# Performance work log

Hardware: AMD Instinct MI355X
Metric: run time of the kernel (lower is better)

## Reference

```python
import jax, jax.numpy as jnp
import numpy as np
import math

B, N, E, H = 2, 4096, 256, 8
HS = E // H  # head_size = 32


def setup_inputs() -> dict:
    key = jax.random.key(0)
    ks = jax.random.split(key, 8)
    s = 1.0 / math.sqrt(E)
    return {
        "node_features": jax.random.normal(ks[0], (B, N, E), dtype=jnp.float32),
        "adj": jax.random.randint(ks[1], (B, N, N), 0, 2).astype(jnp.bool_),
        "Wq": jax.random.normal(ks[2], (E, E), dtype=jnp.float32) * s,
        "bq": jax.random.normal(ks[3], (E,), dtype=jnp.float32) * s,
        "Wk": jax.random.normal(ks[4], (E, E), dtype=jnp.float32) * s,
        "bk": jax.random.normal(ks[5], (E,), dtype=jnp.float32) * s,
        "Wv": jax.random.normal(ks[6], (E, E), dtype=jnp.float32) * s,
        "bv": jax.random.normal(ks[7], (E,), dtype=jnp.float32) * s,
    }


def _split_heads(x):
    # (B, N, E) -> (B, H, N, HS)
    return x.reshape(B, N, H, HS).transpose(0, 2, 1, 3)


def reference(node_features, adj, Wq, bq, Wk, bk, Wv, bv):
    # nn.Linear: x @ W.T + b
    Q = _split_heads(node_features @ Wq.T + bq)
    K = _split_heads(node_features @ Wk.T + bk)
    V = _split_heads(node_features @ Wv.T + bv)
    scores = jnp.einsum("bhnd,bhmd->bhnm", Q, K) / math.sqrt(HS)
    scores = jnp.where(adj[:, None, :, :], scores, -jnp.inf)
    probs = jax.nn.softmax(scores, axis=-1)
    out = jnp.einsum("bhnm,bhmd->bhnd", probs, V)
    # (B, H, N, HS) -> (B, N, E); note: original forward does NOT apply W_out
    return out.transpose(0, 2, 1, 3).reshape(B, N, E)
```

## Files before the change

### kernel.cpp

```cpp
#include <hip/hip_runtime.h>

typedef __attribute__((ext_vector_type(8))) short short8;
typedef __attribute__((ext_vector_type(4))) float f32x4;
typedef __attribute__((ext_vector_type(4))) unsigned short u16x4;

constexpr int cB = 2, cN = 4096, cE = 256, cH = 8, cHS = 32;

__device__ __forceinline__ unsigned short f2bf(float f) {
    unsigned int u = __builtin_bit_cast(unsigned int, f);
    u = (u + 0x7FFFu + ((u >> 16) & 1u)) >> 16;
    return (unsigned short)u;
}

__device__ __forceinline__ unsigned int cvt_pk_bf16(float lo, float hi) {
    unsigned int r;
    asm("v_cvt_pk_bf16_f32 %0, %1, %2" : "=v"(r) : "v"(lo), "v"(hi));
    return r;
}

__global__ __launch_bounds__(256) void cvt_x_kernel(const float* __restrict__ x,
                                                    unsigned short* __restrict__ xb) {
    int t = blockIdx.x * 256 + threadIdx.x;
    f32x4 v = *((const f32x4*)x + t);
    u16x4 o = { f2bf(v[0]), f2bf(v[1]), f2bf(v[2]), f2bf(v[3]) };
    *((u16x4*)xb + t) = o;
}

__global__ __launch_bounds__(256) void cvt_w_kernel(const float* __restrict__ Wq,
                                                    const float* __restrict__ Wk,
                                                    const float* __restrict__ Wv,
                                                    unsigned short* __restrict__ wcb) {
    int t = blockIdx.x * 256 + threadIdx.x;
    int f = t * 4;
    int o = f >> 8, i = f & 255;
    const float* src = (o < 256) ? Wq : (o < 512 ? Wk : Wv);
    f32x4 v = *(const f32x4*)(src + (size_t)(o & 255) * 256 + i);
    u16x4 ov = { f2bf(v[0]), f2bf(v[1]), f2bf(v[2]), f2bf(v[3]) };
    *((u16x4*)wcb + t) = ov;
}

__global__ __launch_bounds__(256) void bitpack_kernel(const int* __restrict__ adj,
                                                      unsigned long long* __restrict__ mask) {
    int lane = threadIdx.x & 63;
    int wave = blockIdx.x * 4 + (threadIdx.x >> 6);
    const int nwaves = 2048 * 4;
    const int nwords = cB * cN * cN / 64;
    for (int w = wave; w < nwords; w += nwaves) {
        int v = adj[(size_t)w * 64 + lane];
        unsigned long long bal = __ballot(v != 0);
        if (lane == 0) mask[w] = bal;
    }
}

__global__ __launch_bounds__(256) void qkv_proj_kernel(const unsigned short* __restrict__ xb,
                                                       const unsigned short* __restrict__ wcb,
                                                       const float* __restrict__ bq,
                                                       const float* __restrict__ bk,
                                                       const float* __restrict__ bv,
                                                       unsigned short* __restrict__ Qb,
                                                       unsigned short* __restrict__ Kb,
                                                       unsigned short* __restrict__ Vt) {
    const int wv = threadIdx.x >> 6, lane = threadIdx.x & 63;
    const int col = lane & 15, grp = lane >> 4;
    const int rowbase = blockIdx.x * 64 + wv * 16;
    const int colbase = blockIdx.y * 64;
    f32x4 acc[4] = {};
    for (int kk = 0; kk < 8; ++kk) {
        short8 a = *(const short8*)(xb + (size_t)(rowbase + col) * 256 + kk * 32 + grp * 8);
        #pragma unroll
        for (int c = 0; c < 4; ++c) {
            short8 bf = *(const short8*)(wcb + (size_t)(colbase + c * 16 + col) * 256 + kk * 32 + grp * 8);
            acc[c] = __builtin_amdgcn_mfma_f32_16x16x32_bf16(a, bf, acc[c], 0, 0, 0);
        }
    }
    #pragma unroll
    for (int c = 0; c < 4; ++c) {
        const int o = colbase + c * 16 + col;
        const int sel = o >> 8, oo = o & 255;
        const float bias = (sel == 0 ? bq : sel == 1 ? bk : bv)[oo];
        const int h = oo >> 5, hs = oo & 31;
        const int R0 = rowbase + grp * 4;
        const int b = R0 >> 12, n0 = R0 & 4095;
        if (sel < 2) {
            unsigned short* dst = (sel == 0) ? Qb : Kb;
            #pragma unroll
            for (int r = 0; r < 4; ++r)
                dst[(size_t)((b * cH + h) * cN + n0 + r) * cHS + hs] = f2bf(acc[c][r] + bias);
        } else {
            unsigned short* vrow = Vt + (size_t)((b * cH + h) * cHS + hs) * cN;
            #pragma unroll
            for (int r = 0; r < 4; ++r) {
                const int n = n0 + r;
                const int pos = (n & ~31) + 2 * (n & 15) + ((n >> 4) & 1);
                vrow[pos] = f2bf(acc[c][r] + bias);
            }
        }
    }
}

__global__ __launch_bounds__(256) void attn_kernel(const unsigned short* __restrict__ Qb,
                                                   const unsigned short* __restrict__ Kb,
                                                   const unsigned short* __restrict__ Vt,
                                                   const unsigned int* __restrict__ mask32,
                                                   float* __restrict__ out) {
    __shared__ unsigned int p_smem[4][2][16][20];
    const int wv = threadIdx.x >> 6, lane = threadIdx.x & 63;
    const int col = lane & 15, grp = lane >> 4;
    int bid = blockIdx.x;
    bid = (bid & 7) * 64 + (bid >> 3);
    const int task = bid * 4 + wv;
    const int qt = task & 127, h = (task >> 7) & 7, b = task >> 10;
    const int qbase = qt * 32;
    const unsigned short* Qh = Qb + (size_t)(b * cH + h) * cN * cHS;
    const unsigned short* Kh = Kb + (size_t)(b * cH + h) * cN * cHS;
    const unsigned short* Vh = Vt + (size_t)(b * cH + h) * cHS * cN;
    const unsigned int* mrow = mask32 + (size_t)(b * cN + qbase) * 128;
    unsigned int (*pb)[16][20] = p_smem[wv];

    short8 aq[2];
    aq[0] = *(const short8*)(Qh + (size_t)(qbase + col) * cHS + grp * 8);
    aq[1] = *(const short8*)(Qh + (size_t)(qbase + 16 + col) * cHS + grp * 8);

    f32x4 acc[2][2] = {};
    float ll[2][4] = {};
    const float CE = 1.4426950408889634f * 0.17677669529663687f;
    const f32x4 z4 = {0.f, 0.f, 0.f, 0.f};

    short8 ck0 = *(const short8*)(Kh + (size_t)col * cHS + grp * 8);
    short8 ck1 = *(const short8*)(Kh + (size_t)(16 + col) * cHS + grp * 8);
    short8 cv0 = *(const short8*)(Vh + (size_t)col * cN + grp * 8);
    short8 cv1 = *(const short8*)(Vh + (size_t)(16 + col) * cN + grp * 8);
    unsigned int cm[8];
    #pragma unroll
    for (int i = 0; i < 8; ++i)
        cm[i] = mrow[(size_t)((i >> 2) * 16 + grp * 4 + (i & 3)) * 128];

    for (int kt = 0; kt < 128; ++kt) {
        const short8 k0 = ck0, k1 = ck1, v0 = cv0, v1 = cv1;
        unsigned int m8[8];
        #pragma unroll
        for (int i = 0; i < 8; ++i) m8[i] = cm[i];
        if (kt < 127) {
            const int kb = (kt + 1) * 32;
            ck0 = *(const short8*)(Kh + (size_t)(kb + col) * cHS + grp * 8);
            ck1 = *(const short8*)(Kh + (size_t)(kb + 16 + col) * cHS + grp * 8);
            cv0 = *(const short8*)(Vh + (size_t)col * cN + kb + grp * 8);
            cv1 = *(const short8*)(Vh + (size_t)(16 + col) * cN + kb + grp * 8);
            #pragma unroll
            for (int i = 0; i < 8; ++i)
                cm[i] = mrow[(size_t)((i >> 2) * 16 + grp * 4 + (i & 3)) * 128 + kt + 1];
        }

        f32x4 s[2][2];
        s[0][0] = __builtin_amdgcn_mfma_f32_16x16x32_bf16(aq[0], k0, z4, 0, 0, 0);
        s[0][1] = __builtin_amdgcn_mfma_f32_16x16x32_bf16(aq[0], k1, z4, 0, 0, 0);
        s[1][0] = __builtin_amdgcn_mfma_f32_16x16x32_bf16(aq[1], k0, z4, 0, 0, 0);
        s[1][1] = __builtin_amdgcn_mfma_f32_16x16x32_bf16(aq[1], k1, z4, 0, 0, 0);

        #pragma unroll
        for (int qs = 0; qs < 2; ++qs) {
            #pragma unroll
            for (int r = 0; r < 4; ++r) {
                const unsigned int w32 = m8[qs * 4 + r];
                float e0 = __builtin_exp2f(s[qs][0][r] * CE);
                float e1 = __builtin_exp2f(s[qs][1][r] * CE);
                e0 = ((w32 >> col) & 1u) ? e0 : 0.f;
                e1 = ((w32 >> (16 + col)) & 1u) ? e1 : 0.f;
                ll[qs][r] += e0 + e1;
                pb[qs][grp * 4 + r][col] = cvt_pk_bf16(e0, e1);
            }
        }
        #pragma unroll
        for (int qs = 0; qs < 2; ++qs) {
            short8 pa = *(const short8*)&pb[qs][col][grp * 4];
            acc[qs][0] = __builtin_amdgcn_mfma_f32_16x16x32_bf16(pa, v0, acc[qs][0], 0, 0, 0);
            acc[qs][1] = __builtin_amdgcn_mfma_f32_16x16x32_bf16(pa, v1, acc[qs][1], 0, 0, 0);
        }
    }

    #pragma unroll
    for (int qs = 0; qs < 2; ++qs) {
        #pragma unroll
        for (int r = 0; r < 4; ++r) {
            float s = ll[qs][r];
            s += __shfl_xor(s, 1);
            s += __shfl_xor(s, 2);
            s += __shfl_xor(s, 4);
            s += __shfl_xor(s, 8);
            const float inv = 1.0f / s;
            const int qrow = qbase + qs * 16 + grp * 4 + r;
            float* op = out + (size_t)(b * cN + qrow) * cE + h * 32;
            op[col]      = acc[qs][0][r] * inv;
            op[16 + col] = acc[qs][1][r] * inv;
        }
    }
}

extern "C" void kernel_launch(void* const* d_in, const int* in_sizes, int n_in,
                              void* d_out, int out_size, void* d_ws, size_t ws_size,
                              hipStream_t stream) {
    const float* x   = (const float*)d_in[0];
    const int*   adj = (const int*)d_in[1];
    const float* Wq  = (const float*)d_in[2];
    const float* bq  = (const float*)d_in[3];
    const float* Wk  = (const float*)d_in[4];
    const float* bk  = (const float*)d_in[5];
    const float* Wv  = (const float*)d_in[6];
    const float* bv  = (const float*)d_in[7];
    float* out = (float*)d_out;

    char* ws = (char*)d_ws;
    unsigned short* Xb  = (unsigned short*)(ws);
    unsigned short* Wcb = (unsigned short*)(ws + (4ull << 20));
    unsigned short* Qb  = (unsigned short*)(ws + (5ull << 20));
    unsigned short* Kb  = (unsigned short*)(ws + (9ull << 20));
    unsigned short* Vt  = (unsigned short*)(ws + (13ull << 20));
    unsigned long long* mask64 = (unsigned long long*)(ws + (17ull << 20));

    cvt_x_kernel<<<dim3(2048), dim3(256), 0, stream>>>(x, Xb);
    cvt_w_kernel<<<dim3(192), dim3(256), 0, stream>>>(Wq, Wk, Wv, Wcb);
    bitpack_kernel<<<dim3(2048), dim3(256), 0, stream>>>(adj, mask64);
    qkv_proj_kernel<<<dim3(128, 12), dim3(256), 0, stream>>>(Xb, Wcb, bq, bk, bv, Qb, Kb, Vt);
    attn_kernel<<<dim3(512), dim3(256), 0, stream>>>(Qb, Kb, Vt, (const unsigned int*)mask64, out);
}
```

Before: 196.1 us.

## Split key range across waves in attention and fold scaling into Q

Each attention block now handles one 32-query tile, and its four waves each take a quarter of the key range. Partial outputs and row sums are combined through shared memory, which quadruples the grid and adds parallelism. The softmax scale is folded into Q during projection, masking becomes a bitwise AND on packed bf16, and row sums are computed by an MFMA against a ones vector instead of scalar adds. The software prefetch of the next K/V/mask tile is removed and replaced with direct loads inside the loop, which risks exposing more memory latency.

```diff
diff --git a/kernel.cpp b/kernel.cpp
--- a/kernel.cpp
+++ b/kernel.cpp
@@ -64,6 +64,7 @@
     const int col = lane & 15, grp = lane >> 4;
     const int rowbase = blockIdx.x * 64 + wv * 16;
     const int colbase = blockIdx.y * 64;
+    const float CE = 1.4426950408889634f * 0.17677669529663687f;
     f32x4 acc[4] = {};
     for (int kk = 0; kk < 8; ++kk) {
         short8 a = *(const short8*)(xb + (size_t)(rowbase + col) * 256 + kk * 32 + grp * 8);
@@ -81,11 +82,14 @@
         const int h = oo >> 5, hs = oo & 31;
         const int R0 = rowbase + grp * 4;
         const int b = R0 >> 12, n0 = R0 & 4095;
-        if (sel < 2) {
-            unsigned short* dst = (sel == 0) ? Qb : Kb;
+        if (sel == 0) {
             #pragma unroll
             for (int r = 0; r < 4; ++r)
-                dst[(size_t)((b * cH + h) * cN + n0 + r) * cHS + hs] = f2bf(acc[c][r] + bias);
+                Qb[(size_t)((b * cH + h) * cN + n0 + r) * cHS + hs] = f2bf((acc[c][r] + bias) * CE);
+        } else if (sel == 1) {
+            #pragma unroll
+            for (int r = 0; r < 4; ++r)
+                Kb[(size_t)((b * cH + h) * cN + n0 + r) * cHS + hs] = f2bf(acc[c][r] + bias);
         } else {
             unsigned short* vrow = Vt + (size_t)((b * cH + h) * cHS + hs) * cN;
             #pragma unroll
@@ -98,101 +102,90 @@
     }
 }
 
-__global__ __launch_bounds__(256) void attn_kernel(const unsigned short* __restrict__ Qb,
-                                                   const unsigned short* __restrict__ Kb,
-                                                   const unsigned short* __restrict__ Vt,
-                                                   const unsigned int* __restrict__ mask32,
-                                                   float* __restrict__ out) {
-    __shared__ unsigned int p_smem[4][2][16][20];
+__global__ __launch_bounds__(256, 5) void attn_kernel(const unsigned short* __restrict__ Qb,
+                                                      const unsigned short* __restrict__ Kb,
+                                                      const unsigned short* __restrict__ Vt,
+                                                      const unsigned int* __restrict__ mask32,
+                                                      float* __restrict__ out) {
+    __shared__ float comb[4][64][24];
     const int wv = threadIdx.x >> 6, lane = threadIdx.x & 63;
     const int col = lane & 15, grp = lane >> 4;
     int bid = blockIdx.x;
-    bid = (bid & 7) * 64 + (bid >> 3);
-    const int task = bid * 4 + wv;
-    const int qt = task & 127, h = (task >> 7) & 7, b = task >> 10;
+    bid = (bid & 7) * 256 + (bid >> 3);
+    const int qt = bid & 127, h = (bid >> 7) & 7, b = bid >> 10;
     const int qbase = qt * 32;
     const unsigned short* Qh = Qb + (size_t)(b * cH + h) * cN * cHS;
     const unsigned short* Kh = Kb + (size_t)(b * cH + h) * cN * cHS;
     const unsigned short* Vh = Vt + (size_t)(b * cH + h) * cHS * cN;
     const unsigned int* mrow = mask32 + (size_t)(b * cN + qbase) * 128;
-    unsigned int (*pb)[16][20] = p_smem[wv];
-
-    short8 aq[2];
-    aq[0] = *(const short8*)(Qh + (size_t)(qbase + col) * cHS + grp * 8);
-    aq[1] = *(const short8*)(Qh + (size_t)(qbase + 16 + col) * cHS + grp * 8);
+    unsigned int* pw = (unsigned int*)&comb[0][0][0] + wv * 640;
+
+    const short8 aq0 = *(const short8*)(Qh + (size_t)(qbase + col) * cHS + grp * 8);
+    const short8 aq1 = *(const short8*)(Qh + (size_t)(qbase + 16 + col) * cHS + grp * 8);
 
     f32x4 acc[2][2] = {};
-    float ll[2][4] = {};
-    const float CE = 1.4426950408889634f * 0.17677669529663687f;
+    f32x4 lacc[2] = {};
     const f32x4 z4 = {0.f, 0.f, 0.f, 0.f};
-
-    short8 ck0 = *(const short8*)(Kh + (size_t)col * cHS + grp * 8);
-    short8 ck1 = *(const short8*)(Kh + (size_t)(16 + col) * cHS + grp * 8);
-    short8 cv0 = *(const short8*)(Vh + (size_t)col * cN + grp * 8);
-    short8 cv1 = *(const short8*)(Vh + (size_t)(16 + col) * cN + grp * 8);
-    unsigned int cm[8];
-    #pragma unroll
-    for (int i = 0; i < 8; ++i)
-        cm[i] = mrow[(size_t)((i >> 2) * 16 + grp * 4 + (i & 3)) * 128];
-
-    for (int kt = 0; kt < 128; ++kt) {
-        const short8 k0 = ck0, k1 = ck1, v0 = cv0, v1 = cv1;
-        unsigned int m8[8];
-        #pragma unroll
-        for (int i = 0; i < 8; ++i) m8[i] = cm[i];
-        if (kt < 127) {
-            const int kb = (kt + 1) * 32;
-            ck0 = *(const short8*)(Kh + (size_t)(kb + col) * cHS + grp * 8);
-            ck1 = *(const short8*)(Kh + (size_t)(kb + 16 + col) * cHS + grp * 8);
-            cv0 = *(const short8*)(Vh + (size_t)col * cN + kb + grp * 8);
-            cv1 = *(const short8*)(Vh + (size_t)(16 + col) * cN + kb + grp * 8);
-            #pragma unroll
-            for (int i = 0; i < 8; ++i)
-                cm[i] = mrow[(size_t)((i >> 2) * 16 + grp * 4 + (i & 3)) * 128 + kt + 1];
-        }
+    const short8 ones = { 0x3F80, 0x3F80, 0x3F80, 0x3F80, 0x3F80, 0x3F80, 0x3F80, 0x3F80 };
+
+    const int ktEnd = wv * 32 + 32;
+    #pragma unroll 1
+    for (int kt = wv * 32; kt < ktEnd; ++kt) {
+        const int kbase = kt * 32;
+        const short8 k0 = *(const short8*)(Kh + (size_t)(kbase + col) * cHS + grp * 8);
+        const short8 k1 = *(const short8*)(Kh + (size_t)(kbase + 16 + col) * cHS + grp * 8);
+        const short8 v0 = *(const short8*)(Vh + (size_t)col * cN + kbase + grp * 8);
+        const short8 v1 = *(const short8*)(Vh + (size_t)(16 + col) * cN + kbase + grp * 8);
 
         f32x4 s[2][2];
-        s[0][0] = __builtin_amdgcn_mfma_f32_16x16x32_bf16(aq[0], k0, z4, 0, 0, 0);
-        s[0][1] = __builtin_amdgcn_mfma_f32_16x16x32_bf16(aq[0], k1, z4, 0, 0, 0);
-        s[1][0] = __builtin_amdgcn_mfma_f32_16x16x32_bf16(aq[1], k0, z4, 0, 0, 0);
-        s[1][1] = __builtin_amdgcn_mfma_f32_16x16x32_bf16(aq[1], k1, z4, 0, 0, 0);
+        s[0][0] = __builtin_amdgcn_mfma_f32_16x16x32_bf16(aq0, k0, z4, 0, 0, 0);
+        s[0][1] = __builtin_amdgcn_mfma_f32_16x16x32_bf16(aq0, k1, z4, 0, 0, 0);
+        s[1][0] = __builtin_amdgcn_mfma_f32_16x16x32_bf16(aq1, k0, z4, 0, 0, 0);
+        s[1][1] = __builtin_amdgcn_mfma_f32_16x16x32_bf16(aq1, k1, z4, 0, 0, 0);
 
         #pragma unroll
         for (int qs = 0; qs < 2; ++qs) {
             #pragma unroll
             for (int r = 0; r < 4; ++r) {
-                const unsigned int w32 = m8[qs * 4 + r];
-                float e0 = __builtin_exp2f(s[qs][0][r] * CE);
-                float e1 = __builtin_exp2f(s[qs][1][r] * CE);
-                e0 = ((w32 >> col) & 1u) ? e0 : 0.f;
-                e1 = ((w32 >> (16 + col)) & 1u) ? e1 : 0.f;
-                ll[qs][r] += e0 + e1;
-                pb[qs][grp * 4 + r][col] = cvt_pk_bf16(e0, e1);
+                const unsigned int w32 = mrow[(size_t)(qs * 16 + grp * 4 + r) * 128 + kt];
+                const float e0 = __builtin_exp2f(s[qs][0][r]);
+                const float e1 = __builtin_exp2f(s[qs][1][r]);
+                const unsigned int msk = ((w32 >> col) & 0x00010001u) * 0xFFFFu;
+                pw[qs * 320 + (grp * 4 + r) * 20 + col] = cvt_pk_bf16(e0, e1) & msk;
             }
         }
         #pragma unroll
         for (int qs = 0; qs < 2; ++qs) {
-            short8 pa = *(const short8*)&pb[qs][col][grp * 4];
+            const short8 pa = *(const short8*)(pw + qs * 320 + col * 20 + grp * 4);
             acc[qs][0] = __builtin_amdgcn_mfma_f32_16x16x32_bf16(pa, v0, acc[qs][0], 0, 0, 0);
             acc[qs][1] = __builtin_amdgcn_mfma_f32_16x16x32_bf16(pa, v1, acc[qs][1], 0, 0, 0);
-        }
-    }
-
+            lacc[qs]   = __builtin_amdgcn_mfma_f32_16x16x32_bf16(pa, ones, lacc[qs], 0, 0, 0);
+        }
+    }
+
+    __syncthreads();
+    float* me = &comb[wv][lane][0];
+    *(f32x4*)(me +  0) = acc[0][0];
+    *(f32x4*)(me +  4) = acc[0][1];
+    *(f32x4*)(me +  8) = acc[1][0];
+    *(f32x4*)(me + 12) = acc[1][1];
+    *(f32x4*)(me + 16) = lacc[0];
+    *(f32x4*)(me + 20) = lacc[1];
+    __syncthreads();
+
+    const int sg = wv, qs = sg >> 1, half = sg & 1;
+    const int grp2 = lane >> 4, col2 = lane & 15;
+    f32x4 a = {0.f, 0.f, 0.f, 0.f};
+    f32x4 l = {0.f, 0.f, 0.f, 0.f};
     #pragma unroll
-    for (int qs = 0; qs < 2; ++qs) {
-        #pragma unroll
-        for (int r = 0; r < 4; ++r) {
-            float s = ll[qs][r];
-            s += __shfl_xor(s, 1);
-            s += __shfl_xor(s, 2);
-            s += __shfl_xor(s, 4);
-            s += __shfl_xor(s, 8);
-            const float inv = 1.0f / s;
-            const int qrow = qbase + qs * 16 + grp * 4 + r;
-            float* op = out + (size_t)(b * cN + qrow) * cE + h * 32;
-            op[col]      = acc[qs][0][r] * inv;
-            op[16 + col] = acc[qs][1][r] * inv;
-        }
+    for (int w = 0; w < 4; ++w) {
+        a += *(const f32x4*)&comb[w][lane][sg * 4];
+        l += *(const f32x4*)&comb[w][lane][16 + qs * 4];
+    }
+    const int row0 = qbase + qs * 16 + grp2 * 4;
+    #pragma unroll
+    for (int j = 0; j < 4; ++j) {
+        out[(size_t)(b * cN + row0 + j) * cE + h * 32 + half * 16 + col2] = a[j] / l[j];
     }
 }
 
@@ -221,5 +214,5 @@
     cvt_w_kernel<<<dim3(192), dim3(256), 0, stream>>>(Wq, Wk, Wv, Wcb);
     bitpack_kernel<<<dim3(2048), dim3(256), 0, stream>>>(adj, mask64);
     qkv_proj_kernel<<<dim3(128, 12), dim3(256), 0, stream>>>(Xb, Wcb, bq, bk, bv, Qb, Kb, Vt);
-    attn_kernel<<<dim3(512), dim3(256), 0, stream>>>(Qb, Kb, Vt, (const unsigned int*)mask64, out);
-}
+    attn_kernel<<<dim3(2048), dim3(256), 0, stream>>>(Qb, Kb, Vt, (const unsigned int*)mask64, out);
+}
```

Measured after the change: 180.9 us. 1.08x faster.
